# Optimization experiments

Hardware: AMD Instinct MI355X
Metric: run time of the kernel (lower is better)

## Reference

```python
import jax, jax.numpy as jnp
import numpy as np

B, N, D, H, L, R = 2, 2048, 1024, 16, 3, 2
HID = int(D * 2.67)
NASH_ITERS, SINK_ITERS = 3, 10
EPS = 1e-6


def _rmsnorm(x, w):
    return x * w * jax.lax.rsqrt(jnp.mean(x * x, axis=-1, keepdims=True) + EPS)


def _sinkhorn(logits):
    # Sinkhorn-Knopp projection of exp(logits) to a doubly-stochastic matrix
    M = jnp.exp(logits)
    for _ in range(SINK_ITERS):
        M = M / jnp.sum(M, axis=1, keepdims=True)
        M = M / jnp.sum(M, axis=0, keepdims=True)
    return M


def _swiglu(x, wg, wu, wd):
    return (jax.nn.silu(x @ wg) * (x @ wu)) @ wd


def _attention(xl, wq, wk, Wv):
    # causal multi-head attention at one scale; V projection (Wv) is shared across scales
    b, n, d = xl.shape
    dh = d // H
    q = (xl @ wq).reshape(b, n, H, dh)
    k = (xl @ wk).reshape(b, n, H, dh)
    v = (xl @ Wv).reshape(b, n, H, dh)
    scores = jnp.einsum('bqhd,bkhd->bhqk', q, k) / jnp.asarray(float(np.sqrt(dh)), xl.dtype)
    mask = jnp.tril(jnp.ones((n, n), bool))
    scores = jnp.where(mask, scores, jnp.asarray(-1e9, xl.dtype))
    p = jax.nn.softmax(scores, axis=-1)
    return jnp.einsum('bhqk,bkhd->bqhd', p, v).reshape(b, n, d)


def _forward(x, norm_attn_w, norm_ffn_w, W_dec, Wq, Wk, Wv, Wo, agg_logits,
             w_gate, w_up, w_down, mhc_attn_logits, mhc_ffn_logits):
    residual = x
    xn = _rmsnorm(x, norm_attn_w)
    # 1) hierarchical decomposition: avg-pool by R each level, per-scale projection
    scales = []
    cur = xn
    for l in range(L):
        scales.append(cur @ W_dec[l])
        if l < L - 1:
            b, n, d = cur.shape
            cur = cur.reshape(b, n // R, R, d).mean(axis=2)
    # 2) multiscale causal attention with shared V; upsample back to N and project
    outs = []
    for l in range(L):
        o = _attention(scales[l], Wq[l], Wk[l], Wv)
        o = jnp.repeat(o, R ** l, axis=1)  # [B, N, D]
        outs.append(o @ Wo)
    Y = jnp.stack(outs, axis=0)  # [L, B, N, D]
    # 3) Nash aggregation: best-response iterations on scale weights
    w = jax.nn.softmax(agg_logits)
    for _ in range(NASH_ITERS):
        y_bar = jnp.einsum('l,lbnd->bnd', w, Y)
        u = -jnp.mean((Y - y_bar[None]) ** 2, axis=(1, 2, 3))  # [L] payoffs
        w = jax.nn.softmax(agg_logits + u)
    attn_out = jnp.einsum('l,lbnd->bnd', w, Y)
    aux_loss = jnp.sum(w * jnp.log(w * L + 1e-9))  # KL(w || uniform)
    # 4) mHC residual mixing (attention branch): doubly-stochastic convex mix
    P = _sinkhorn(mhc_attn_logits)
    x = P[0, 0] * residual + P[0, 1] * attn_out
    # 5) SwiGLU FFN + mHC residual (FFN branch)
    residual = x
    xn = _rmsnorm(x, norm_ffn_w)
    ffn_out = _swiglu(xn, w_gate, w_up, w_down)
    P2 = _sinkhorn(mhc_ffn_logits)
    x = P2[0, 0] * residual + P2[0, 1] * ffn_out
    return x, aux_loss


def setup_inputs() -> dict:
    key = jax.random.key(0)
    ks = jax.random.split(key, 16)
    init = 0.02
    s = lambda i, shape: jax.random.normal(ks[i], shape, jnp.float32) * init
    return {
        'x': jax.random.normal(ks[0], (B, N, D), jnp.float32),
        'norm_attn_w': jnp.ones((D,), jnp.float32),
        'norm_ffn_w': jnp.ones((D,), jnp.float32),
        'W_dec': s(1, (L, D, D)),
        'Wq': s(2, (L, D, D)),
        'Wk': s(3, (L, D, D)),
        'Wv': s(4, (D, D)),
        'Wo': s(5, (D, D)),
        'agg_logits': jnp.zeros((L,), jnp.float32),
        'w_gate': s(6, (D, HID)),
        'w_up': s(7, (D, HID)),
        'w_down': s(8, (HID, D)),
        'mhc_attn_logits': jnp.zeros((2, 2), jnp.float32),
        'mhc_ffn_logits': jnp.zeros((2, 2), jnp.float32),
    }


def reference(x, norm_attn_w, norm_ffn_w, W_dec, Wq, Wk, Wv, Wo, agg_logits,
              w_gate, w_up, w_down, mhc_attn_logits, mhc_ffn_logits):
    return _forward(x, norm_attn_w, norm_ffn_w, W_dec, Wq, Wk, Wv, Wo, agg_logits,
                    w_gate, w_up, w_down, mhc_attn_logits, mhc_ffn_logits)
```

## Files before the change

kernel.cpp:

```cpp
#include <hip/hip_runtime.h>
#include <stdint.h>


#define B_   2
#define N_   2048
#define D_   1024
#define H_   16
#define DH_  64
#define HID_ 2734
#define HIDP 2816
#define CNT  (B_*N_*D_)
#define LOG2E 1.4426950408889634f

typedef unsigned short u16;
typedef __attribute__((ext_vector_type(8))) short short8;
typedef __attribute__((ext_vector_type(4))) float f32x4;
typedef __attribute__((ext_vector_type(4))) uint16_t u16x4;

__device__ __forceinline__ u16 f2bf(float f) {
  uint32_t u = __builtin_bit_cast(uint32_t, f);
  u += 0x7fffu + ((u >> 16) & 1u);
  return (u16)(u >> 16);
}
__device__ __forceinline__ float bf2f(u16 h) {
  uint32_t u = ((uint32_t)h) << 16;
  return __builtin_bit_cast(float, u);
}
__device__ __forceinline__ uint32_t pkbf(float a, float b) {
  return (uint32_t)f2bf(a) | ((uint32_t)f2bf(b) << 16);
}
__device__ __forceinline__ void gload_lds16(const void* g, void* l) {
  __builtin_amdgcn_global_load_lds(
      (const __attribute__((address_space(1))) uint32_t*)g,
      (__attribute__((address_space(3))) uint32_t*)l, 16, 0, 0);
}

__global__ __launch_bounds__(256) void twconv_k(const float* __restrict__ W, u16* __restrict__ BT,
                                                int K, int N, int KP, int NP, float scale) {
  __shared__ float t[32][33];
  const int tx = threadIdx.x & 31, ty = threadIdx.x >> 5;
  const int nb = blockIdx.x * 32, kb = blockIdx.y * 32;
  #pragma unroll
  for (int i = 0; i < 4; i++) {
    int k = kb + ty + i*8, n = nb + tx;
    t[ty + i*8][tx] = (k < K && n < N) ? W[(size_t)k * N + n] * scale : 0.f;
  }
  __syncthreads();
  #pragma unroll
  for (int i = 0; i < 4; i++) {
    int n = nb + ty + i*8, k = kb + tx;
    if (n < NP && k < KP) BT[(size_t)n * KP + k] = f2bf(t[tx][ty + i*8]);
  }
}

__global__ __launch_bounds__(256) void conv_k(const float* __restrict__ in, u16* __restrict__ out, int total) {
  for (int i = blockIdx.x*256 + threadIdx.x; i < total; i += gridDim.x*256)
    out[i] = f2bf(in[i]);
}

__global__ __launch_bounds__(256) void rmsnorm_k(const float* __restrict__ x,
                                                 const float* __restrict__ w,
                                                 u16* __restrict__ out) {
  const int row = blockIdx.x;
  const float* xr = x + (size_t)row * D_;
  float ss = 0.f;
  #pragma unroll
  for (int i = 0; i < 4; i++) { float v = xr[threadIdx.x + i*256]; ss += v*v; }
  ss += __shfl_xor(ss, 1);  ss += __shfl_xor(ss, 2);  ss += __shfl_xor(ss, 4);
  ss += __shfl_xor(ss, 8);  ss += __shfl_xor(ss, 16); ss += __shfl_xor(ss, 32);
  __shared__ float red[4];
  if ((threadIdx.x & 63) == 0) red[threadIdx.x >> 6] = ss;
  __syncthreads();
  float sc = rsqrtf((red[0]+red[1]+red[2]+red[3]) * (1.f/D_) + 1e-6f);
  #pragma unroll
  for (int i = 0; i < 4; i++) {
    int c = threadIdx.x + i*256;
    out[(size_t)row * D_ + c] = f2bf(xr[c] * w[c] * sc);
  }
}

__global__ __launch_bounds__(256) void pool_k(const u16* __restrict__ in, u16* __restrict__ out, int lg) {
  const int No = 1 << lg;
  const int total4 = B_ * No * 256;
  for (int i = blockIdx.x*256 + threadIdx.x; i < total4; i += gridDim.x*256) {
    int d4 = i & 255; int j = (i >> 8) & (No - 1); int b = i >> (8 + lg);
    size_t src = ((size_t)(b*2*No + 2*j) << 10) + d4*4;
    u16x4 a = *(const u16x4*)(in + src);
    u16x4 c = *(const u16x4*)(in + src + 1024);
    u16x4 o;
    #pragma unroll
    for (int t = 0; t < 4; t++) o[t] = f2bf(0.5f * (bf2f(a[t]) + bf2f(c[t])));
    *(u16x4*)(out + (size_t)i*4) = o;
  }
}

template<int MT, int MODE>
__global__ __launch_bounds__(256) void gemm_t(const u16* __restrict__ A, const u16* __restrict__ BT,
                                              void* __restrict__ Cv, const float* __restrict__ X1,
                                              const float* __restrict__ SCp,
                                              int N, int K, int t1, int t2, unsigned int bt_stride) {
  __shared__ __align__(16) u16 As[MT*32*32];
  __shared__ __align__(16) u16 Bs[128*32];
  const int tid = threadIdx.x;
  const int lane = tid & 63, wid = tid >> 6;
  const int quad = lane >> 4, c16 = lane & 15;
  const int y = blockIdx.y;
  const int m0 = y * (MT*32), n0 = blockIdx.x * 128;
  const int wm = wid >> 1, wn = wid & 1;
  const int level = (y >= t2) ? 2 : ((y >= t1) ? 1 : 0);
  BT += (size_t)level * bt_stride;

  f32x4 acc[MT][4];
  #pragma unroll
  for (int i = 0; i < MT; i++)
    #pragma unroll
    for (int j = 0; j < 4; j++) acc[i][j] = f32x4{0.f,0.f,0.f,0.f};

  const int srow = lane >> 2;
  const int schunk = lane & 3;
  for (int k0 = 0; k0 < K; k0 += 32) {
    #pragma unroll
    for (int t = 0; t < MT/2; t++) {
      int idx = wid*(MT/2) + t;
      int row = idx*16 + srow;
      int g = (schunk ^ ((row >> 1) & 3)) * 8;
      gload_lds16(A + (size_t)(m0+row)*K + k0 + g, As + idx*512);
    }
    #pragma unroll
    for (int t = 0; t < 2; t++) {
      int idx = wid*2 + t;
      int row = idx*16 + srow;
      int g = (schunk ^ ((row >> 1) & 3)) * 8;
      gload_lds16(BT + (size_t)(n0+row)*K + k0 + g, Bs + idx*512);
    }
    __syncthreads();
    short8 af[MT], bfr[4];
    #pragma unroll
    for (int mt = 0; mt < MT; mt++) {
      int ar = wm*(MT*16) + mt*16 + c16;
      af[mt]  = *(const short8*)(As + ar*32 + (quad ^ ((ar>>1)&3))*8);
    }
    #pragma unroll
    for (int nt = 0; nt < 4; nt++) {
      int br = wn*64 + nt*16 + c16;
      bfr[nt] = *(const short8*)(Bs + br*32 + (quad ^ ((br>>1)&3))*8);
    }
    #pragma unroll
    for (int mt = 0; mt < MT; mt++)
      #pragma unroll
      for (int nt = 0; nt < 4; nt++)
        acc[mt][nt] = __builtin_amdgcn_mfma_f32_16x16x32_bf16(af[mt], bfr[nt], acc[mt][nt], 0, 0, 0);
    __syncthreads();
  }
  if (MODE == 1) {
    u16* C = (u16*)Cv;
    #pragma unroll
    for (int mt = 0; mt < MT; mt++)
      #pragma unroll
      for (int nt = 0; nt < 4; nt++)
        #pragma unroll
        for (int r = 0; r < 4; r++) {
          int row = m0 + wm*(MT*16) + mt*16 + quad*4 + r;
          int col = n0 + wn*64 + nt*16 + c16;
          C[(size_t)row * N + col] = f2bf(acc[mt][nt][r]);
        }
  } else {
    float* C = (float*)Cv;
    const float q0 = SCp[11], q1 = SCp[12];
    #pragma unroll
    for (int mt = 0; mt < MT; mt++)
      #pragma unroll
      for (int nt = 0; nt < 4; nt++)
        #pragma unroll
        for (int r = 0; r < 4; r++) {
          int row = m0 + wm*(MT*16) + mt*16 + quad*4 + r;
          int col = n0 + wn*64 + nt*16 + c16;
          size_t o = (size_t)row * N + col;
          C[o] = q0 * X1[o] + q1 * acc[mt][nt][r];
        }
  }
}

__global__ __launch_bounds__(256) void vtrans_k(const u16* __restrict__ in, u16* __restrict__ out, int Nl) {
  __shared__ u16 t[32][33];
  const int n0 = blockIdx.x*32, c0 = blockIdx.y*32, b = blockIdx.z;
  const int tx = threadIdx.x & 31, ty = threadIdx.x >> 5;
  #pragma unroll
  for (int i = 0; i < 4; i++)
    t[ty + i*8][tx] = in[(size_t)(b*Nl + n0 + ty + i*8)*3072 + c0 + tx];
  __syncthreads();
  #pragma unroll
  for (int i = 0; i < 4; i++)
    out[(size_t)(b*1024 + c0 + ty + i*8)*Nl + n0 + tx] = t[tx][ty + i*8];
}

__global__ __launch_bounds__(256) void flash_k(const u16* __restrict__ QKVg,
                                               const u16* __restrict__ VTg,
                                               u16* __restrict__ Og) {
  __shared__ __align__(16) u16 Kt[2][64*64];
  __shared__ __align__(16) u16 Vt[2][64*64];
  __shared__ __align__(16) u16 Ps[4][32*68];
  const int tid = threadIdx.x, lane = tid & 63, wid = tid >> 6;
  const int quad = lane >> 4, c16 = lane & 15;
  const int id = blockIdx.x;
  int qt, bh, Nl, rowbase; size_t vtoff;
  if (id < 512)      { qt = 15 - (id >> 5);            bh = id & 31;  Nl = 2048; rowbase = 0;    vtoff = 0; }
  else if (id < 768) { int t2 = id - 512; qt = 7 - (t2 >> 5); bh = t2 & 31; Nl = 1024; rowbase = 4096; vtoff = 4194304; }
  else               { int t2 = id - 768; qt = 3 - (t2 >> 5); bh = t2 & 31; Nl = 512;  rowbase = 6144; vtoff = 6291456; }
  const int b = bh >> 4, h = bh & 15;
  const u16* QK = QKVg + ((size_t)(rowbase + b*Nl)) * 3072 + h*64;
  u16* Ow = Og + ((size_t)(rowbase + b*Nl)) * 1024 + h*64;
  const u16* VT = VTg + vtoff + ((size_t)b*1024 + h*64) * (size_t)Nl;

  const int q0r = qt*128 + wid*32;
  short8 bq[2][2];
  #pragma unroll
  for (int qh = 0; qh < 2; qh++) {
    const u16* qp = QK + (size_t)(q0r + qh*16 + c16)*3072 + quad*8;
    bq[qh][0] = *(const short8*)qp;
    bq[qh][1] = *(const short8*)(qp + 32);
  }
  const int si0 = wid*2, si1 = si0 + 1;
  const int sr0 = si0*8 + (lane>>3), sr1 = si1*8 + (lane>>3);
  const int sg  = ((lane&7) ^ (lane>>3)) * 8;
  const u16* Ks0 = QK + 1024 + (size_t)sr0*3072 + sg;
  const u16* Ks1 = QK + 1024 + (size_t)sr1*3072 + sg;
  const u16* Vs0 = VT + (size_t)sr0*Nl + sg;
  const u16* Vs1 = VT + (size_t)sr1*Nl + sg;

  f32x4 oacc[2][4];
  f32x4 lacc[2];
  #pragma unroll
  for (int qh = 0; qh < 2; qh++) {
    lacc[qh] = f32x4{0.f,0.f,0.f,0.f};
    #pragma unroll
    for (int nt = 0; nt < 4; nt++) oacc[qh][nt] = f32x4{0.f,0.f,0.f,0.f};
  }

  auto stage = [&](int kt, int p) {
    const size_t ko = (size_t)kt * 64;
    gload_lds16(Ks0 + ko*3072, &Kt[p][si0*512]);
    gload_lds16(Ks1 + ko*3072, &Kt[p][si1*512]);
    gload_lds16(Vs0 + ko,      &Vt[p][si0*512]);
    gload_lds16(Vs1 + ko,      &Vt[p][si1*512]);
  };
  const int kmax_w = 2*qt + (wid >> 1);
  const int ktot   = 2*qt + 2;
  stage(0, 0);

  for (int kt = 0; kt < ktot; kt++) {
    const int p = kt & 1;
    __syncthreads();
    if (kt + 1 < ktot) stage(kt+1, p^1);
    if (kt > kmax_w) continue;

    f32x4 st[2][4];
    #pragma unroll
    for (int nt = 0; nt < 4; nt++) {
      int key = nt*16 + c16, x = key & 7;
      short8 a0 = *(const short8*)(&Kt[p][key*64 + ((quad    ) ^ x)*8]);
      short8 a1 = *(const short8*)(&Kt[p][key*64 + ((quad + 4) ^ x)*8]);
      #pragma unroll
      for (int qh = 0; qh < 2; qh++) {
        f32x4 s = f32x4{0.f,0.f,0.f,0.f};
        s = __builtin_amdgcn_mfma_f32_16x16x32_bf16(a0, bq[qh][0], s, 0, 0, 0);
        s = __builtin_amdgcn_mfma_f32_16x16x32_bf16(a1, bq[qh][1], s, 0, 0, 0);
        st[qh][nt] = s;
      }
    }
    if (kt >= 2*qt) {
      const int kb = kt*64;
      #pragma unroll
      for (int qh = 0; qh < 2; qh++) {
        const int qr = q0r + qh*16 + c16;
        #pragma unroll
        for (int nt = 0; nt < 4; nt++) {
          #pragma unroll
          for (int r = 0; r < 4; r++) {
            float e = __builtin_amdgcn_exp2f(st[qh][nt][r]);
            st[qh][nt][r] = (kb + nt*16 + quad*4 + r <= qr) ? e : 0.f;
          }
          lacc[qh] += st[qh][nt];
        }
      }
    } else {
      #pragma unroll
      for (int qh = 0; qh < 2; qh++)
        #pragma unroll
        for (int nt = 0; nt < 4; nt++) {
          #pragma unroll
          for (int r = 0; r < 4; r++) st[qh][nt][r] = __builtin_amdgcn_exp2f(st[qh][nt][r]);
          lacc[qh] += st[qh][nt];
        }
    }
    #pragma unroll
    for (int qh = 0; qh < 2; qh++) {
      const int prow = qh*16 + c16;
      #pragma unroll
      for (int nt = 0; nt < 4; nt++) {
        uint2 pk;
        pk.x = pkbf(st[qh][nt][0], st[qh][nt][1]);
        pk.y = pkbf(st[qh][nt][2], st[qh][nt][3]);
        *(uint2*)(&Ps[wid][prow*68 + nt*16 + quad*4]) = pk;
      }
    }
    short8 bp[2][2];
    #pragma unroll
    for (int qh = 0; qh < 2; qh++) {
      bp[qh][0] = *(const short8*)(&Ps[wid][(qh*16 + c16)*68 +      quad*8]);
      bp[qh][1] = *(const short8*)(&Ps[wid][(qh*16 + c16)*68 + 32 + quad*8]);
    }
    #pragma unroll
    for (int nt = 0; nt < 4; nt++) {
      int dh = nt*16 + c16, x = dh & 7;
      short8 a0 = *(const short8*)(&Vt[p][dh*64 + ((quad    ) ^ x)*8]);
      short8 a1 = *(const short8*)(&Vt[p][dh*64 + ((quad + 4) ^ x)*8]);
      #pragma unroll
      for (int qh = 0; qh < 2; qh++) {
        oacc[qh][nt] = __builtin_amdgcn_mfma_f32_16x16x32_bf16(a0, bp[qh][0], oacc[qh][nt], 0, 0, 0);
        oacc[qh][nt] = __builtin_amdgcn_mfma_f32_16x16x32_bf16(a1, bp[qh][1], oacc[qh][nt], 0, 0, 0);
      }
    }
  }
  #pragma unroll
  for (int qh = 0; qh < 2; qh++) {
    float ls = lacc[qh][0] + lacc[qh][1] + lacc[qh][2] + lacc[qh][3];
    ls += __shfl_xor(ls, 16);
    ls += __shfl_xor(ls, 32);
    const float rl = 1.f / ls;
    #pragma unroll
    for (int nt = 0; nt < 4; nt++) {
      uint2 o;
      o.x = pkbf(oacc[qh][nt][0]*rl, oacc[qh][nt][1]*rl);
      o.y = pkbf(oacc[qh][nt][2]*rl, oacc[qh][nt][3]*rl);
      *(uint2*)(Ow + (size_t)(q0r + qh*16 + c16)*1024 + nt*16 + quad*4) = o;
    }
  }
}

__global__ __launch_bounds__(256) void gram_k(const u16* __restrict__ Y0, const u16* __restrict__ Y1,
                                              const u16* __restrict__ Y2, float* __restrict__ G) {
  float a[6] = {0,0,0,0,0,0};
  const int total4 = CNT/4;
  for (int i = blockIdx.x*256 + threadIdx.x; i < total4; i += gridDim.x*256) {
    int d4 = i & 255; int n = (i >> 8) & (N_-1); int b = i >> 19;
    u16x4 y0v = *(const u16x4*)(Y0 + (size_t)i*4);
    u16x4 y1v = *(const u16x4*)(Y1 + (((size_t)(b*1024 + (n>>1))) << 10) + d4*4);
    u16x4 y2v = *(const u16x4*)(Y2 + (((size_t)(b*512  + (n>>2))) << 10) + d4*4);
    #pragma unroll
    for (int t = 0; t < 4; t++) {
      float y0 = bf2f(y0v[t]), y1 = bf2f(y1v[t]), y2 = bf2f(y2v[t]);
      a[0] += y0*y0; a[1] += y0*y1; a[2] += y0*y2;
      a[3] += y1*y1; a[4] += y1*y2; a[5] += y2*y2;
    }
  }
  __shared__ float red[4][6];
  const int lane = threadIdx.x & 63, wid = threadIdx.x >> 6;
  #pragma unroll
  for (int t = 0; t < 6; t++) {
    float v = a[t];
    v += __shfl_xor(v, 1);  v += __shfl_xor(v, 2);  v += __shfl_xor(v, 4);
    v += __shfl_xor(v, 8);  v += __shfl_xor(v, 16); v += __shfl_xor(v, 32);
    a[t] = v;
  }
  if (lane == 0)
    #pragma unroll
    for (int t = 0; t < 6; t++) red[wid][t] = a[t];
  __syncthreads();
  if (threadIdx.x < 6)
    atomicAdd(&G[threadIdx.x], red[0][threadIdx.x] + red[1][threadIdx.x] +
                               red[2][threadIdx.x] + red[3][threadIdx.x]);
}

__global__ void zero_k(float* p) { if (threadIdx.x < 64) p[threadIdx.x] = 0.f; }

__global__ void head_k(float* SC, const float* __restrict__ agg, const float* __restrict__ mA,
                       const float* __restrict__ mF, float* __restrict__ aux_out) {
  if (threadIdx.x != 0 || blockIdx.x != 0) return;
  float G[6];
  for (int t = 0; t < 6; t++) G[t] = SC[t];
  const int gi[3][3] = {{0,1,2},{1,3,4},{2,4,5}};
  float a[3] = {agg[0], agg[1], agg[2]};
  float w[3];
  {
    float m = fmaxf(a[0], fmaxf(a[1], a[2])); float s = 0.f;
    for (int l = 0; l < 3; l++) { w[l] = expf(a[l]-m); s += w[l]; }
    for (int l = 0; l < 3; l++) w[l] /= s;
  }
  const float inv = 1.f / (float)CNT;
  for (int it = 0; it < 3; it++) {
    float q = 0.f;
    for (int l = 0; l < 3; l++) for (int m2 = 0; m2 < 3; m2++) q += w[l]*w[m2]*G[gi[l][m2]];
    float z[3];
    for (int l = 0; l < 3; l++) {
      float dot = w[0]*G[gi[l][0]] + w[1]*G[gi[l][1]] + w[2]*G[gi[l][2]];
      z[l] = a[l] - (G[gi[l][l]] - 2.f*dot + q) * inv;
    }
    float m = fmaxf(z[0], fmaxf(z[1], z[2])); float s = 0.f;
    for (int l = 0; l < 3; l++) { w[l] = expf(z[l]-m); s += w[l]; }
    for (int l = 0; l < 3; l++) w[l] /= s;
  }
  SC[6] = w[0]; SC[7] = w[1]; SC[8] = w[2];
  aux_out[0] = w[0]*logf(w[0]*3.f + 1e-9f) + w[1]*logf(w[1]*3.f + 1e-9f) + w[2]*logf(w[2]*3.f + 1e-9f);
  for (int which = 0; which < 2; which++) {
    const float* Lg = which ? mF : mA;
    float M0 = expf(Lg[0]), M1 = expf(Lg[1]), M2 = expf(Lg[2]), M3 = expf(Lg[3]);
    for (int i2 = 0; i2 < 10; i2++) {
      float r0 = M0+M1, r1 = M2+M3; M0 /= r0; M1 /= r0; M2 /= r1; M3 /= r1;
      float c0 = M0+M2, c1 = M1+M3; M0 /= c0; M2 /= c0; M1 /= c1; M3 /= c1;
    }
    SC[9 + which*2] = M0; SC[10 + which*2] = M1;
  }
}

__global__ __launch_bounds__(256) void mix1_k(const float4* __restrict__ x, const u16* __restrict__ Y0,
                                              const u16* __restrict__ Y1, const u16* __restrict__ Y2,
                                              const float* __restrict__ SC, float4* __restrict__ x1) {
  const float w0 = SC[6], w1 = SC[7], w2 = SC[8], p0 = SC[9], p1 = SC[10];
  const int total4 = CNT/4;
  for (int i = blockIdx.x*256 + threadIdx.x; i < total4; i += gridDim.x*256) {
    int d4 = i & 255; int n = (i >> 8) & (N_-1); int b = i >> 19;
    u16x4 y0v = *(const u16x4*)(Y0 + (size_t)i*4);
    u16x4 y1v = *(const u16x4*)(Y1 + (((size_t)(b*1024 + (n>>1))) << 10) + d4*4);
    u16x4 y2v = *(const u16x4*)(Y2 + (((size_t)(b*512  + (n>>2))) << 10) + d4*4);
    float4 xv = x[i];
    float4 o;
    o.x = p0*xv.x + p1*(w0*bf2f(y0v[0]) + w1*bf2f(y1v[0]) + w2*bf2f(y2v[0]));
    o.y = p0*xv.y + p1*(w0*bf2f(y0v[1]) + w1*bf2f(y1v[1]) + w2*bf2f(y2v[1]));
    o.z = p0*xv.z + p1*(w0*bf2f(y0v[2]) + w1*bf2f(y1v[2]) + w2*bf2f(y2v[2]));
    o.w = p0*xv.w + p1*(w0*bf2f(y0v[3]) + w1*bf2f(y1v[3]) + w2*bf2f(y2v[3]));
    x1[i] = o;
  }
}

__global__ __launch_bounds__(256) void silumul_k(const u16* __restrict__ gu, u16* __restrict__ h) {
  const int total4 = 4096 * 704;
  for (int t = blockIdx.x*256 + threadIdx.x; t < total4; t += gridDim.x*256) {
    int row = t / 704, c4 = (t - row*704) * 4;
    u16x4 g4 = *(const u16x4*)(gu + (size_t)row*5632 + c4);
    u16x4 u4 = *(const u16x4*)(gu + (size_t)row*5632 + 2816 + c4);
    u16x4 o;
    #pragma unroll
    for (int j = 0; j < 4; j++) {
      float gv = bf2f(g4[j]), uv = bf2f(u4[j]);
      o[j] = f2bf(gv / (1.f + __expf(-gv)) * uv);
    }
    *(u16x4*)(h + (size_t)row*2816 + c4) = o;
  }
}

extern "C" void kernel_launch(void* const* d_in, const int* in_sizes, int n_in,
                              void* d_out, int out_size, void* d_ws, size_t ws_size,
                              hipStream_t stream) {
  (void)in_sizes; (void)n_in; (void)out_size; (void)ws_size;
  const float* x    = (const float*)d_in[0];
  const float* nw1  = (const float*)d_in[1];
  const float* nw2  = (const float*)d_in[2];
  const float* Wdec = (const float*)d_in[3];
  const float* Wq   = (const float*)d_in[4];
  const float* Wk   = (const float*)d_in[5];
  const float* Wv   = (const float*)d_in[6];
  const float* Wo   = (const float*)d_in[7];
  const float* agg  = (const float*)d_in[8];
  const float* Wg   = (const float*)d_in[9];
  const float* Wu   = (const float*)d_in[10];
  const float* Wdn  = (const float*)d_in[11];
  const float* mA   = (const float*)d_in[12];
  const float* mF   = (const float*)d_in[13];
  float* out = (float*)d_out;

  char* ws = (char*)d_ws;
  size_t off = 0;
  auto take = [&](size_t b) { size_t r = off; off += (b + 255) & ~(size_t)255; return r; };

  u16* A_wp  = (u16*)(ws + take((size_t)9216*1024*2));
  u16* WdecB = (u16*)(ws + take((size_t)3*1024*1024*2));
  u16* Wqkv  = (u16*)(ws + take((size_t)9216*1024*2));
  u16* BTgu  = (u16*)(ws + take((size_t)5632*1024*2));
  u16* WdnT  = (u16*)(ws + take((size_t)HIDP*1024*2));
  u16* WoT   = (u16*)(ws + take((size_t)1024*1024*2));
  u16* xn_all = (u16*)(ws + take((size_t)7168*1024*2));
  float* x1  = (float*)(ws + take((size_t)CNT*4));
  float* SCb = (float*)(ws + take(256));
  char*  big = ws + take(88080384);
  u16*   QKV   = (u16*)big;
  u16*   VTa   = (u16*)(big + 44040192);
  u16*   Ob    = (u16*)(big + 58720256);
  u16*   YC    = (u16*)(big + 73400320);
  u16*   gu    = (u16*)big;
  u16*   hbuf  = (u16*)(big + 46137344);

  const int rowbase[3] = {0, 4096, 6144};
  const int Nl[3] = {2048, 1024, 512};
  const size_t vtoff[3] = {0, 4194304, 6291456};

  dim3 blk(256);
  const int BIG = 1 << 30;

  conv_k<<<2048, blk, 0, stream>>>(Wdec, WdecB, 3*1024*1024);
  for (int l = 0; l < 3; l++) {
    twconv_k<<<dim3(32,32), blk, 0, stream>>>(Wq + (size_t)l*1048576, A_wp + (size_t)(l*3072 + 0)*1024,
                                              1024,1024,1024,1024, 0.125f * LOG2E);
    twconv_k<<<dim3(32,32), blk, 0, stream>>>(Wk + (size_t)l*1048576, A_wp + (size_t)(l*3072 + 1024)*1024,
                                              1024,1024,1024,1024, 1.f);
    twconv_k<<<dim3(32,32), blk, 0, stream>>>(Wv, A_wp + (size_t)(l*3072 + 2048)*1024,
                                              1024,1024,1024,1024, 1.f);
  }
  twconv_k<<<dim3(32,32), blk, 0, stream>>>(Wo, WoT, 1024,1024,1024,1024, 1.f);
  twconv_k<<<dim3(88,32), blk, 0, stream>>>(Wg,  BTgu,                     1024, HID_, 1024, HIDP, 1.f);
  twconv_k<<<dim3(88,32), blk, 0, stream>>>(Wu,  BTgu + (size_t)HIDP*1024, 1024, HID_, 1024, HIDP, 1.f);
  twconv_k<<<dim3(32,88), blk, 0, stream>>>(Wdn, WdnT, HID_, 1024, HIDP, 1024, 1.f);
  gemm_t<4,1><<<dim3(8, 72), blk, 0, stream>>>(A_wp, WdecB, Wqkv, nullptr, nullptr,
                                               1024, 1024, 24, 48, 1024u*1024u);

  rmsnorm_k<<<4096, blk, 0, stream>>>(x, nw1, xn_all);
  pool_k<<<1024, blk, 0, stream>>>(xn_all,                      xn_all + (size_t)4096*1024, 10);
  pool_k<<<512,  blk, 0, stream>>>(xn_all + (size_t)4096*1024,  xn_all + (size_t)6144*1024, 9);

  gemm_t<4,1><<<dim3(24, 56), blk, 0, stream>>>(xn_all, Wqkv, QKV, nullptr, nullptr,
                                                3072, 1024, 32, 48, 3072u*1024u);
  for (int l = 0; l < 3; l++)
    vtrans_k<<<dim3(Nl[l]/32, 32, B_), blk, 0, stream>>>(QKV + (size_t)rowbase[l]*3072 + 2048,
                                                         VTa + vtoff[l], Nl[l]);
  flash_k<<<896, blk, 0, stream>>>(QKV, VTa, Ob);
  gemm_t<2,1><<<dim3(8, 112), blk, 0, stream>>>(Ob, WoT, YC, nullptr, nullptr,
                                                1024, 1024, BIG, BIG, 0u);

  u16* YC1 = YC + (size_t)4096*1024;
  u16* YC2 = YC + (size_t)6144*1024;
  zero_k<<<1, 64, 0, stream>>>(SCb);
  gram_k<<<1024, blk, 0, stream>>>(YC, YC1, YC2, SCb);
  head_k<<<1, 64, 0, stream>>>(SCb, agg, mA, mF, out + CNT);
  mix1_k<<<2048, blk, 0, stream>>>((const float4*)x, YC, YC1, YC2, SCb, (float4*)x1);

  rmsnorm_k<<<4096, blk, 0, stream>>>(x1, nw2, xn_all);
  gemm_t<4,1><<<dim3(44, 32), blk, 0, stream>>>(xn_all, BTgu, gu, nullptr, nullptr,
                                                5632, 1024, BIG, BIG, 0u);
  silumul_k<<<2048, blk, 0, stream>>>(gu, hbuf);
  gemm_t<2,2><<<dim3(8, 64), blk, 0, stream>>>(hbuf, WdnT, out, x1, SCb,
                                               1024, HIDP, BIG, BIG, 0u);
}
```

Baseline: 562.5 us.

## Fuse weight prep, rmsnorm+pool, mix+rmsnorm, and SiLU into GEMM epilogue

All weight conversion and transpose kernels, plus the zeroing of the scratch scalars, are merged into one large launch. Gate and up weight rows are interleaved in 16-column groups so the gate/up GEMM epilogue can apply SiLU and the multiply directly and write h, which removes the separate gu buffer and its pass. The first rmsnorm now also produces the first pooled level, the aggregation mix is fused with the second rmsnorm, and the three V-transpose launches become one. These cut launch count and intermediate memory traffic, at the cost of branchier kernels and higher register pressure in the GEMM epilogue.

```diff
diff --git a/kernel.cpp b/kernel.cpp
--- a/kernel.cpp
+++ b/kernel.cpp
@@ -35,47 +35,89 @@
       (__attribute__((address_space(3))) uint32_t*)l, 16, 0, 0);
 }
 
-__global__ __launch_bounds__(256) void twconv_k(const float* __restrict__ W, u16* __restrict__ BT,
-                                                int K, int N, int KP, int NP, float scale) {
-  __shared__ float t[32][33];
+__global__ __launch_bounds__(256) void wprep_k(const float* __restrict__ Wdec, const float* __restrict__ Wq,
+                                               const float* __restrict__ Wk, const float* __restrict__ Wv,
+                                               const float* __restrict__ Wo, const float* __restrict__ Wg,
+                                               const float* __restrict__ Wu, const float* __restrict__ Wdn,
+                                               u16* __restrict__ A_wp, u16* __restrict__ WdecB,
+                                               u16* __restrict__ WoT, u16* __restrict__ BTgu,
+                                               u16* __restrict__ WdnT, float* __restrict__ SCb) {
+  const int bid = blockIdx.x;
+  if (bid >= 18688) {
+    if (bid == 18688 && threadIdx.x < 64) SCb[threadIdx.x] = 0.f;
+    int i = (bid - 18688)*1024 + threadIdx.x*4;
+    float4 v = *(const float4*)(Wdec + i);
+    u16x4 o; o[0]=f2bf(v.x); o[1]=f2bf(v.y); o[2]=f2bf(v.z); o[3]=f2bf(v.w);
+    *(u16x4*)(WdecB + i) = o;
+    return;
+  }
+  const float* src; u16* dst; int K, N, KP; float scale; int imode; int bx, by;
+  if (bid < 9216) {
+    int j = bid >> 10, t = bid & 1023; bx = t & 31; by = t >> 5;
+    int l = j / 3, which = j - l*3;
+    src = which==0 ? Wq + (size_t)l*1048576 : which==1 ? Wk + (size_t)l*1048576 : Wv;
+    dst = A_wp + (size_t)(l*3072 + which*1024)*1024;
+    K = 1024; N = 1024; KP = 1024; scale = (which==0) ? 0.125f*LOG2E : 1.f; imode = 0;
+  } else if (bid < 10240) {
+    int t = bid - 9216; bx = t & 31; by = t >> 5;
+    src = Wo; dst = WoT; K=1024; N=1024; KP=1024; scale=1.f; imode=0;
+  } else if (bid < 13056) {
+    int t = bid - 10240; bx = t % 88; by = t / 88;
+    src = Wg; dst = BTgu; K=1024; N=HID_; KP=1024; scale=1.f; imode=1;
+  } else if (bid < 15872) {
+    int t = bid - 13056; bx = t % 88; by = t / 88;
+    src = Wu; dst = BTgu; K=1024; N=HID_; KP=1024; scale=1.f; imode=2;
+  } else {
+    int t = bid - 15872; bx = t & 31; by = t >> 5;
+    src = Wdn; dst = WdnT; K=HID_; N=1024; KP=HIDP; scale=1.f; imode=0;
+  }
+  __shared__ float tt[32][33];
   const int tx = threadIdx.x & 31, ty = threadIdx.x >> 5;
-  const int nb = blockIdx.x * 32, kb = blockIdx.y * 32;
+  const int nb = bx*32, kb = by*32;
   #pragma unroll
   for (int i = 0; i < 4; i++) {
     int k = kb + ty + i*8, n = nb + tx;
-    t[ty + i*8][tx] = (k < K && n < N) ? W[(size_t)k * N + n] * scale : 0.f;
+    tt[ty + i*8][tx] = (k < K && n < N) ? src[(size_t)k * N + n] * scale : 0.f;
   }
   __syncthreads();
   #pragma unroll
   for (int i = 0; i < 4; i++) {
     int n = nb + ty + i*8, k = kb + tx;
-    if (n < NP && k < KP) BT[(size_t)n * KP + k] = f2bf(t[tx][ty + i*8]);
-  }
-}
-
-__global__ __launch_bounds__(256) void conv_k(const float* __restrict__ in, u16* __restrict__ out, int total) {
-  for (int i = blockIdx.x*256 + threadIdx.x; i < total; i += gridDim.x*256)
-    out[i] = f2bf(in[i]);
-}
-
-__global__ __launch_bounds__(256) void rmsnorm_k(const float* __restrict__ x,
-                                                 const float* __restrict__ w,
-                                                 u16* __restrict__ out) {
-  const int row = blockIdx.x;
-  const float* xr = x + (size_t)row * D_;
-  float ss = 0.f;
-  #pragma unroll
-  for (int i = 0; i < 4; i++) { float v = xr[threadIdx.x + i*256]; ss += v*v; }
-  ss += __shfl_xor(ss, 1);  ss += __shfl_xor(ss, 2);  ss += __shfl_xor(ss, 4);
-  ss += __shfl_xor(ss, 8);  ss += __shfl_xor(ss, 16); ss += __shfl_xor(ss, 32);
-  __shared__ float red[4];
-  if ((threadIdx.x & 63) == 0) red[threadIdx.x >> 6] = ss;
-  __syncthreads();
-  float sc = rsqrtf((red[0]+red[1]+red[2]+red[3]) * (1.f/D_) + 1e-6f);
+    int r;
+    if (imode == 0) r = n;
+    else if (imode == 1) r = ((n>>4)<<5) + (n&15);
+    else r = ((n>>4)<<5) + 16 + (n&15);
+    dst[(size_t)r * KP + k] = f2bf(tt[tx][ty + i*8]);
+  }
+}
+
+__global__ __launch_bounds__(256) void rmsA_k(const float* __restrict__ x, const float* __restrict__ w,
+                                              u16* __restrict__ xn, u16* __restrict__ xp1) {
+  const int j = blockIdx.x;
+  const float* xr0 = x + (size_t)(2*j) * D_;
+  const float* xr1 = xr0 + D_;
+  float a0[4], a1[4], wv[4];
+  float ss0 = 0.f, ss1 = 0.f;
   #pragma unroll
   for (int i = 0; i < 4; i++) {
     int c = threadIdx.x + i*256;
-    out[(size_t)row * D_ + c] = f2bf(xr[c] * w[c] * sc);
+    a0[i] = xr0[c]; a1[i] = xr1[c]; wv[i] = w[c];
+    ss0 += a0[i]*a0[i]; ss1 += a1[i]*a1[i];
+  }
+  #pragma unroll
+  for (int o = 1; o < 64; o <<= 1) { ss0 += __shfl_xor(ss0, o); ss1 += __shfl_xor(ss1, o); }
+  __shared__ float r0[4], r1[4];
+  if ((threadIdx.x & 63) == 0) { r0[threadIdx.x >> 6] = ss0; r1[threadIdx.x >> 6] = ss1; }
+  __syncthreads();
+  float sc0 = rsqrtf((r0[0]+r0[1]+r0[2]+r0[3]) * (1.f/D_) + 1e-6f);
+  float sc1 = rsqrtf((r1[0]+r1[1]+r1[2]+r1[3]) * (1.f/D_) + 1e-6f);
+  #pragma unroll
+  for (int i = 0; i < 4; i++) {
+    int c = threadIdx.x + i*256;
+    float xa = a0[i]*wv[i]*sc0, xb = a1[i]*wv[i]*sc1;
+    xn[(size_t)(2*j)*D_ + c]     = f2bf(xa);
+    xn[(size_t)(2*j)*D_ + D_ + c] = f2bf(xb);
+    xp1[(size_t)j*D_ + c] = f2bf(0.5f*(xa + xb));
   }
 }
 
@@ -164,7 +206,7 @@
           int col = n0 + wn*64 + nt*16 + c16;
           C[(size_t)row * N + col] = f2bf(acc[mt][nt][r]);
         }
-  } else {
+  } else if (MODE == 2) {
     float* C = (float*)Cv;
     const float q0 = SCp[11], q1 = SCp[12];
     #pragma unroll
@@ -178,12 +220,41 @@
           size_t o = (size_t)row * N + col;
           C[o] = q0 * X1[o] + q1 * acc[mt][nt][r];
         }
-  }
-}
-
-__global__ __launch_bounds__(256) void vtrans_k(const u16* __restrict__ in, u16* __restrict__ out, int Nl) {
+  } else {
+    u16* Hc = (u16*)Cv;
+    const int hbase = (n0 >> 1) + wn*32;
+    #pragma unroll
+    for (int mt = 0; mt < MT; mt++)
+      #pragma unroll
+      for (int r = 0; r < 4; r++) {
+        int row = m0 + wm*(MT*16) + mt*16 + quad*4 + r;
+        #pragma unroll
+        for (int pr = 0; pr < 2; pr++) {
+          float g = acc[mt][2*pr][r], u = acc[mt][2*pr+1][r];
+          float h = g / (1.f + __expf(-g)) * u;
+          Hc[(size_t)row * HIDP + hbase + pr*16 + c16] = f2bf(h);
+        }
+      }
+  }
+}
+
+__global__ __launch_bounds__(256) void vtrans_k(const u16* __restrict__ QKV, u16* __restrict__ VTa) {
   __shared__ u16 t[32][33];
-  const int n0 = blockIdx.x*32, c0 = blockIdx.y*32, b = blockIdx.z;
+  const int bid = blockIdx.x;
+  int level, tt2;
+  if (bid < 4096)      { level = 0; tt2 = bid; }
+  else if (bid < 6144) { level = 1; tt2 = bid - 4096; }
+  else                 { level = 2; tt2 = bid - 6144; }
+  const int Nl = 2048 >> level;
+  const int ntiles = Nl >> 5;
+  const int b = tt2 / (ntiles*32);
+  const int rem = tt2 - b*(ntiles*32);
+  const int c0 = (rem / ntiles) * 32;
+  const int n0 = (rem - (rem / ntiles)*ntiles) * 32;
+  const int rowbase = (level==0) ? 0 : (level==1) ? 4096 : 6144;
+  const size_t vtoff = (level==0) ? 0 : (level==1) ? 4194304 : 6291456;
+  const u16* in = QKV + (size_t)rowbase*3072 + 2048;
+  u16* out = VTa + vtoff;
   const int tx = threadIdx.x & 31, ty = threadIdx.x >> 5;
   #pragma unroll
   for (int i = 0; i < 4; i++)
@@ -372,8 +443,6 @@
                                red[2][threadIdx.x] + red[3][threadIdx.x]);
 }
 
-__global__ void zero_k(float* p) { if (threadIdx.x < 64) p[threadIdx.x] = 0.f; }
-
 __global__ void head_k(float* SC, const float* __restrict__ agg, const float* __restrict__ mA,
                        const float* __restrict__ mF, float* __restrict__ aux_out) {
   if (threadIdx.x != 0 || blockIdx.x != 0) return;
@@ -413,39 +482,36 @@
   }
 }
 
-__global__ __launch_bounds__(256) void mix1_k(const float4* __restrict__ x, const u16* __restrict__ Y0,
-                                              const u16* __restrict__ Y1, const u16* __restrict__ Y2,
-                                              const float* __restrict__ SC, float4* __restrict__ x1) {
-  const float w0 = SC[6], w1 = SC[7], w2 = SC[8], p0 = SC[9], p1 = SC[10];
-  const int total4 = CNT/4;
-  for (int i = blockIdx.x*256 + threadIdx.x; i < total4; i += gridDim.x*256) {
-    int d4 = i & 255; int n = (i >> 8) & (N_-1); int b = i >> 19;
-    u16x4 y0v = *(const u16x4*)(Y0 + (size_t)i*4);
-    u16x4 y1v = *(const u16x4*)(Y1 + (((size_t)(b*1024 + (n>>1))) << 10) + d4*4);
-    u16x4 y2v = *(const u16x4*)(Y2 + (((size_t)(b*512  + (n>>2))) << 10) + d4*4);
-    float4 xv = x[i];
-    float4 o;
-    o.x = p0*xv.x + p1*(w0*bf2f(y0v[0]) + w1*bf2f(y1v[0]) + w2*bf2f(y2v[0]));
-    o.y = p0*xv.y + p1*(w0*bf2f(y0v[1]) + w1*bf2f(y1v[1]) + w2*bf2f(y2v[1]));
-    o.z = p0*xv.z + p1*(w0*bf2f(y0v[2]) + w1*bf2f(y1v[2]) + w2*bf2f(y2v[2]));
-    o.w = p0*xv.w + p1*(w0*bf2f(y0v[3]) + w1*bf2f(y1v[3]) + w2*bf2f(y2v[3]));
-    x1[i] = o;
-  }
-}
-
-__global__ __launch_bounds__(256) void silumul_k(const u16* __restrict__ gu, u16* __restrict__ h) {
-  const int total4 = 4096 * 704;
-  for (int t = blockIdx.x*256 + threadIdx.x; t < total4; t += gridDim.x*256) {
-    int row = t / 704, c4 = (t - row*704) * 4;
-    u16x4 g4 = *(const u16x4*)(gu + (size_t)row*5632 + c4);
-    u16x4 u4 = *(const u16x4*)(gu + (size_t)row*5632 + 2816 + c4);
-    u16x4 o;
-    #pragma unroll
-    for (int j = 0; j < 4; j++) {
-      float gv = bf2f(g4[j]), uv = bf2f(u4[j]);
-      o[j] = f2bf(gv / (1.f + __expf(-gv)) * uv);
-    }
-    *(u16x4*)(h + (size_t)row*2816 + c4) = o;
+__global__ __launch_bounds__(256) void mixrms_k(const float* __restrict__ x, const u16* __restrict__ Y0,
+                                                const u16* __restrict__ Y1, const u16* __restrict__ Y2,
+                                                const float* __restrict__ SC, const float* __restrict__ w2,
+                                                float* __restrict__ x1, u16* __restrict__ xn2) {
+  const float w0 = SC[6], w1 = SC[7], ww2 = SC[8], p0 = SC[9], p1 = SC[10];
+  const int i = blockIdx.x;
+  const int b = i >> 11, n = i & 2047;
+  const float* xr = x + (size_t)i * D_;
+  const u16* y0 = Y0 + (size_t)i * D_;
+  const u16* y1 = Y1 + (size_t)(b*1024 + (n>>1)) * D_;
+  const u16* y2 = Y2 + (size_t)(b*512  + (n>>2)) * D_;
+  float xv[4], wv[4];
+  float ss = 0.f;
+  #pragma unroll
+  for (int t = 0; t < 4; t++) {
+    int c = threadIdx.x + t*256;
+    float v = p0*xr[c] + p1*(w0*bf2f(y0[c]) + w1*bf2f(y1[c]) + ww2*bf2f(y2[c]));
+    xv[t] = v; wv[t] = w2[c]; ss += v*v;
+    x1[(size_t)i*D_ + c] = v;
+  }
+  #pragma unroll
+  for (int o = 1; o < 64; o <<= 1) ss += __shfl_xor(ss, o);
+  __shared__ float red[4];
+  if ((threadIdx.x & 63) == 0) red[threadIdx.x >> 6] = ss;
+  __syncthreads();
+  float sc = rsqrtf((red[0]+red[1]+red[2]+red[3]) * (1.f/D_) + 1e-6f);
+  #pragma unroll
+  for (int t = 0; t < 4; t++) {
+    int c = threadIdx.x + t*256;
+    xn2[(size_t)i*D_ + c] = f2bf(xv[t]*wv[t]*sc);
   }
 }
 
@@ -487,56 +553,30 @@
   u16*   VTa   = (u16*)(big + 44040192);
   u16*   Ob    = (u16*)(big + 58720256);
   u16*   YC    = (u16*)(big + 73400320);
-  u16*   gu    = (u16*)big;
-  u16*   hbuf  = (u16*)(big + 46137344);
-
-  const int rowbase[3] = {0, 4096, 6144};
-  const int Nl[3] = {2048, 1024, 512};
-  const size_t vtoff[3] = {0, 4194304, 6291456};
+  u16*   hbuf  = (u16*)big;
 
   dim3 blk(256);
   const int BIG = 1 << 30;
 
-  conv_k<<<2048, blk, 0, stream>>>(Wdec, WdecB, 3*1024*1024);
-  for (int l = 0; l < 3; l++) {
-    twconv_k<<<dim3(32,32), blk, 0, stream>>>(Wq + (size_t)l*1048576, A_wp + (size_t)(l*3072 + 0)*1024,
-                                              1024,1024,1024,1024, 0.125f * LOG2E);
-    twconv_k<<<dim3(32,32), blk, 0, stream>>>(Wk + (size_t)l*1048576, A_wp + (size_t)(l*3072 + 1024)*1024,
-                                              1024,1024,1024,1024, 1.f);
-    twconv_k<<<dim3(32,32), blk, 0, stream>>>(Wv, A_wp + (size_t)(l*3072 + 2048)*1024,
-                                              1024,1024,1024,1024, 1.f);
-  }
-  twconv_k<<<dim3(32,32), blk, 0, stream>>>(Wo, WoT, 1024,1024,1024,1024, 1.f);
-  twconv_k<<<dim3(88,32), blk, 0, stream>>>(Wg,  BTgu,                     1024, HID_, 1024, HIDP, 1.f);
-  twconv_k<<<dim3(88,32), blk, 0, stream>>>(Wu,  BTgu + (size_t)HIDP*1024, 1024, HID_, 1024, HIDP, 1.f);
-  twconv_k<<<dim3(32,88), blk, 0, stream>>>(Wdn, WdnT, HID_, 1024, HIDP, 1024, 1.f);
+  wprep_k<<<21760, blk, 0, stream>>>(Wdec, Wq, Wk, Wv, Wo, Wg, Wu, Wdn,
+                                     A_wp, WdecB, WoT, BTgu, WdnT, SCb);
   gemm_t<4,1><<<dim3(8, 72), blk, 0, stream>>>(A_wp, WdecB, Wqkv, nullptr, nullptr,
                                                1024, 1024, 24, 48, 1024u*1024u);
-
-  rmsnorm_k<<<4096, blk, 0, stream>>>(x, nw1, xn_all);
-  pool_k<<<1024, blk, 0, stream>>>(xn_all,                      xn_all + (size_t)4096*1024, 10);
-  pool_k<<<512,  blk, 0, stream>>>(xn_all + (size_t)4096*1024,  xn_all + (size_t)6144*1024, 9);
-
+  rmsA_k<<<2048, blk, 0, stream>>>(x, nw1, xn_all, xn_all + (size_t)4096*1024);
+  pool_k<<<512, blk, 0, stream>>>(xn_all + (size_t)4096*1024, xn_all + (size_t)6144*1024, 9);
   gemm_t<4,1><<<dim3(24, 56), blk, 0, stream>>>(xn_all, Wqkv, QKV, nullptr, nullptr,
                                                 3072, 1024, 32, 48, 3072u*1024u);
-  for (int l = 0; l < 3; l++)
-    vtrans_k<<<dim3(Nl[l]/32, 32, B_), blk, 0, stream>>>(QKV + (size_t)rowbase[l]*3072 + 2048,
-                                                         VTa + vtoff[l], Nl[l]);
+  vtrans_k<<<7168, blk, 0, stream>>>(QKV, VTa);
   flash_k<<<896, blk, 0, stream>>>(QKV, VTa, Ob);
   gemm_t<2,1><<<dim3(8, 112), blk, 0, stream>>>(Ob, WoT, YC, nullptr, nullptr,
                                                 1024, 1024, BIG, BIG, 0u);
-
   u16* YC1 = YC + (size_t)4096*1024;
   u16* YC2 = YC + (size_t)6144*1024;
-  zero_k<<<1, 64, 0, stream>>>(SCb);
   gram_k<<<1024, blk, 0, stream>>>(YC, YC1, YC2, SCb);
   head_k<<<1, 64, 0, stream>>>(SCb, agg, mA, mF, out + CNT);
-  mix1_k<<<2048, blk, 0, stream>>>((const float4*)x, YC, YC1, YC2, SCb, (float4*)x1);
-
-  rmsnorm_k<<<4096, blk, 0, stream>>>(x1, nw2, xn_all);
-  gemm_t<4,1><<<dim3(44, 32), blk, 0, stream>>>(xn_all, BTgu, gu, nullptr, nullptr,
+  mixrms_k<<<4096, blk, 0, stream>>>(x, YC, YC1, YC2, SCb, nw2, x1, xn_all);
+  gemm_t<4,3><<<dim3(44, 32), blk, 0, stream>>>(xn_all, BTgu, hbuf, nullptr, nullptr,
                                                 5632, 1024, BIG, BIG, 0u);
-  silumul_k<<<2048, blk, 0, stream>>>(gu, hbuf);
   gemm_t<2,2><<<dim3(8, 64), blk, 0, stream>>>(hbuf, WdnT, out, x1, SCb,
                                                1024, HIDP, BIG, BIG, 0u);
 }
```

Measured after the change: 505.0 us. 10.2% less time.
